# Kernel tuning notes

Hardware: AMD Instinct MI355X
Metric: run time of the kernel (lower is better)

## Reference

```python
import jax, jax.numpy as jnp
import numpy as np

NUM_NODES = 1_000_000
MEM = 128
NODE_F = 172
EDGE_F = 172
EMB = 128
DECAY = 0.1
B = 16384


def setup_inputs() -> dict:
    key = jax.random.key(0)
    ks = jax.random.split(key, 32)
    g = lambda k, sh, s=0.05: (s * jax.random.normal(k, sh)).astype(jnp.float32)
    inp = {
        "src_ids": jax.random.randint(ks[0], (B,), 0, NUM_NODES),
        "dst_ids": jax.random.randint(ks[1], (B,), 0, NUM_NODES),
        "src_features": g(ks[2], (B, NODE_F), 1.0),
        "dst_features": g(ks[3], (B, NODE_F), 1.0),
        "timestamps": jax.random.uniform(ks[4], (B,), jnp.float32),
        "edge_features": g(ks[5], (B, EDGE_F), 1.0),
        # persistent state (pre-populated so decay math is non-trivial)
        "memory0": g(ks[6], (NUM_NODES, MEM), 1.0),
        "last_update0": jax.random.uniform(ks[7], (NUM_NODES,), jnp.float32),
        # edge_embedding
        "W_edge": g(ks[8], (EDGE_F, MEM)), "b_edge": jnp.zeros((MEM,), jnp.float32),
        # message_processor: Linear(MEM,MEM) -> relu -> Linear(MEM,MEM)
        "W_mp1": g(ks[9], (MEM, MEM)), "b_mp1": jnp.zeros((MEM,), jnp.float32),
        "W_mp2": g(ks[10], (MEM, MEM)), "b_mp2": jnp.zeros((MEM,), jnp.float32),
        # GRUCell(MEM, MEM), torch layout [3*MEM, MEM] (r,z,n)
        "W_ih": g(ks[11], (3 * MEM, MEM)), "W_hh": g(ks[12], (3 * MEM, MEM)),
        "b_ih": jnp.zeros((3 * MEM,), jnp.float32), "b_hh": jnp.zeros((3 * MEM,), jnp.float32),
        # node_embedding
        "W_node": g(ks[13], (NODE_F, MEM)), "b_node": jnp.zeros((MEM,), jnp.float32),
        # embedding_projection: Linear(2*MEM, EMB) -> relu -> Linear(EMB, EMB)
        "W_p1": g(ks[14], (2 * MEM, EMB)), "b_p1": jnp.zeros((EMB,), jnp.float32),
        "W_p2": g(ks[15], (EMB, EMB)), "b_p2": jnp.zeros((EMB,), jnp.float32),
        # link_predictor: Linear(2*EMB, EMB) -> relu -> Linear(EMB, 1) -> sigmoid
        "W_l1": g(ks[16], (2 * EMB, EMB)), "b_l1": jnp.zeros((EMB,), jnp.float32),
        "W_l2": g(ks[17], (EMB, 1)), "b_l2": jnp.zeros((1,), jnp.float32),
    }
    return inp


def _gru_cell(x, h, W_ih, W_hh, b_ih, b_hh):
    gi = x @ W_ih.T + b_ih
    gh = h @ W_hh.T + b_hh
    i_r, i_z, i_n = jnp.split(gi, 3, axis=-1)
    h_r, h_z, h_n = jnp.split(gh, 3, axis=-1)
    r = jax.nn.sigmoid(i_r + h_r)
    z = jax.nn.sigmoid(i_z + h_z)
    n = jnp.tanh(i_n + r * h_n)
    return (1.0 - z) * n + z * h


def reference(src_ids, dst_ids, src_features, dst_features, timestamps, edge_features,
              memory0, last_update0,
              W_edge, b_edge, W_mp1, b_mp1, W_mp2, b_mp2,
              W_ih, W_hh, b_ih, b_hh, W_node, b_node,
              W_p1, b_p1, W_p2, b_p2, W_l1, b_l1, W_l2, b_l2):
    pos = jnp.arange(B, dtype=jnp.int32)

    def update_memory(memory, last_update, ids, messages, ts):
        # batched version of the torch per-row GRU loop: current memory is
        ids = jnp.clip(ids, 0, NUM_NODES - 1)
        proc = jax.nn.relu(messages @ W_mp1 + b_mp1) @ W_mp2 + b_mp2
        dt = jnp.maximum(ts - last_update[ids], 0.0)
        cur = memory[ids] * jnp.exp(-DECAY * dt)[:, None]          # decayed get_memory
        new = _gru_cell(proc, cur, W_ih, W_hh, b_ih, b_hh)          # [B, MEM]
        last_occ = jnp.full((NUM_NODES,), -1, jnp.int32).at[ids].max(pos)
        win = last_occ[ids] == pos
        wids = jnp.where(win, ids, NUM_NODES)                       # OOB rows dropped
        memory = memory.at[wids].set(new, mode="drop")
        last_update = last_update.at[wids].set(ts, mode="drop")
        # torch does updates under no_grad into non-trainable Parameters
        return jax.lax.stop_gradient(memory), jax.lax.stop_gradient(last_update)

    def compute_embeddings(memory, last_update, ids, feats, ts):
        ids = jnp.clip(ids, 0, NUM_NODES - 1)
        dt = jnp.maximum(ts - last_update[ids], 0.0)
        score = jnp.exp(-DECAY * dt)
        mem = memory[ids] * score[:, None]       # get_memory (decayed)
        attended = mem * score[:, None]          # temporal_attention decays again (faithful)
        node_emb = feats @ W_node + b_node
        comb = jnp.concatenate([attended, node_emb], axis=1)
        emb = jax.nn.relu(comb @ W_p1 + b_p1) @ W_p2 + b_p2
        return emb, score

    edge_emb = edge_features @ W_edge + b_edge
    memory, last_update = update_memory(memory0, last_update0, src_ids, edge_emb, timestamps)
    memory, last_update = update_memory(memory, last_update, dst_ids, edge_emb, timestamps)

    src_emb, src_score = compute_embeddings(memory, last_update, src_ids, src_features, timestamps)
    dst_emb, dst_score = compute_embeddings(memory, last_update, dst_ids, dst_features, timestamps)

    link = jnp.concatenate([src_emb, dst_emb], axis=1)
    link_probs = jax.nn.sigmoid(jax.nn.relu(link @ W_l1 + b_l1) @ W_l2 + b_l2)  # [B, 1]
    return link_probs, src_score, dst_score
```

## Files before the change

### kernel.cpp

```cpp
#include <hip/hip_runtime.h>
#include <hip/hip_bf16.h>

#define B_ROWS 16384
#define NODE_F 172
#define MEMD 128
#define NN 1000000

typedef __bf16 bf16;
typedef __bf16 bf16x8 __attribute__((ext_vector_type(8)));
typedef float f32x4 __attribute__((ext_vector_type(4)));

#define W_EDGE_O 0
#define W_MP1_O  24576
#define W_MP2_O  40960
#define W_IH_O   57344
#define W_HH_O   106496
#define W_NODE_O 155648
#define W_P1_O   180224
#define W_P2_O   212992
#define W_L1_O   229376
#define W_TOTAL  262144

__device__ __forceinline__ f32x4 mfma16(bf16x8 a, bf16x8 b, f32x4 c) {
    return __builtin_amdgcn_mfma_f32_16x16x32_bf16(a, b, c, 0, 0, 0);
}

__device__ __forceinline__ int clampid(int id) {
    return id < 0 ? 0 : (id > NN - 1 ? NN - 1 : id);
}

__device__ __forceinline__ float sigmoidf_(float x) {
    return 1.f / (1.f + __expf(-x));
}

__device__ __forceinline__ float tanhf_(float x) {
    return 1.f - 2.f / (__expf(2.f * x) + 1.f);
}

template<int NT, int KSTEPS>
__device__ __forceinline__ void gemm_wave(const bf16* Alds, int lda,
                                          const bf16* Bw, int ldb,
                                          f32x4* acc)
{
    int lane = threadIdx.x & 63;
    int p = lane & 15, q = lane >> 4;
    const bf16* ap  = Alds + p * lda + q * 8;
    const bf16* bp0 = Bw + (long)p * ldb + q * 8;
#pragma unroll
    for (int kt = 0; kt < KSTEPS; ++kt) {
        bf16x8 a = *(const bf16x8*)(ap + kt * 32);
#pragma unroll
        for (int j = 0; j < NT; ++j) {
            bf16x8 b = *(const bf16x8*)(bp0 + (long)j * 16 * ldb + kt * 32);
            acc[j] = mfma16(a, b, acc[j]);
        }
    }
}

__global__ __launch_bounds__(256) void prep_kernel(
    const float* __restrict__ W_edge, const float* __restrict__ W_mp1,
    const float* __restrict__ W_mp2, const float* __restrict__ W_ih,
    const float* __restrict__ W_hh, const float* __restrict__ W_node,
    const float* __restrict__ W_p1, const float* __restrict__ W_p2,
    const float* __restrict__ W_l1,
    int* __restrict__ occS, int* __restrict__ occD, bf16* __restrict__ wb)
{
    int gid = blockIdx.x * 256 + threadIdx.x;
    if (gid < NN / 4) {
        int4 m1 = {-1, -1, -1, -1};
        ((int4*)occS)[gid] = m1;
        ((int4*)occD)[gid] = m1;
    }
    int t = gid;
    if (t < W_TOTAL) {
        float v;
        if (t < W_MP1_O)      { int u = t;            int n = u / 192, k = u % 192; v = (k < NODE_F) ? W_edge[k * 128 + n] : 0.f; }
        else if (t < W_MP2_O) { int u = t - W_MP1_O;  int n = u / 128, k = u % 128; v = W_mp1[k * 128 + n]; }
        else if (t < W_IH_O)  { int u = t - W_MP2_O;  int n = u / 128, k = u % 128; v = W_mp2[k * 128 + n]; }
        else if (t < W_HH_O)  { int u = t - W_IH_O;   v = W_ih[u]; }
        else if (t < W_NODE_O){ int u = t - W_HH_O;   v = W_hh[u]; }
        else if (t < W_P1_O)  { int u = t - W_NODE_O; int n = u / 192, k = u % 192; v = (k < NODE_F) ? W_node[k * 128 + n] : 0.f; }
        else if (t < W_P2_O)  { int u = t - W_P1_O;   int n = u / 256, k = u % 256; v = W_p1[k * 128 + n]; }
        else if (t < W_L1_O)  { int u = t - W_P2_O;   int n = u / 128, k = u % 128; v = W_p2[k * 128 + n]; }
        else                  { int u = t - W_L1_O;   int n = u / 256, k = u % 256; v = W_l1[k * 128 + n]; }
        wb[t] = (bf16)v;
    }
}

__global__ __launch_bounds__(256) void proc_kernel(
    const float* __restrict__ edgef, const bf16* __restrict__ wb,
    const float* __restrict__ b_edge, const float* __restrict__ b_mp1,
    const float* __restrict__ b_mp2, const int* __restrict__ src_ids,
    const int* __restrict__ dst_ids, int* __restrict__ occS,
    int* __restrict__ occD, bf16* __restrict__ procB)
{
    __shared__ bf16 A0[64 * 200];
    __shared__ bf16 A1[64 * 136];
    __shared__ bf16 A2[64 * 136];
    int tid = threadIdx.x;
    long row0 = (long)blockIdx.x * 64;
    if (tid < 64) {
        int rid = (int)row0 + tid;
        atomicMax(&occS[clampid(src_ids[rid])], rid);
        atomicMax(&occD[clampid(dst_ids[rid])], rid);
    }
    {
        int r0 = tid >> 6, c0 = tid & 63;
        for (int r = r0; r < 64; r += 4)
            for (int c = c0; c < 192; c += 64)
                A0[r * 200 + c] = (c < NODE_F) ? (bf16)edgef[(row0 + r) * NODE_F + c] : (bf16)0.f;
    }
    __syncthreads();
    int w = tid >> 6, lane = tid & 63, p = lane & 15, q = lane >> 4;
    f32x4 acc[8];
    for (int j = 0; j < 8; ++j) acc[j] = (f32x4){0.f, 0.f, 0.f, 0.f};
    gemm_wave<8, 6>(A0 + (w * 16) * 200, 200, wb + W_EDGE_O, 192, acc);
    for (int j = 0; j < 8; ++j) {
        int col = j * 16 + p;
        float bb = b_edge[col];
        for (int v = 0; v < 4; ++v)
            A1[(w * 16 + q * 4 + v) * 136 + col] = (bf16)(acc[j][v] + bb);
    }
    __syncthreads();
    for (int j = 0; j < 8; ++j) acc[j] = (f32x4){0.f, 0.f, 0.f, 0.f};
    gemm_wave<8, 4>(A1 + (w * 16) * 136, 136, wb + W_MP1_O, 128, acc);
    for (int j = 0; j < 8; ++j) {
        int col = j * 16 + p;
        float bb = b_mp1[col];
        for (int v = 0; v < 4; ++v)
            A2[(w * 16 + q * 4 + v) * 136 + col] = (bf16)fmaxf(acc[j][v] + bb, 0.f);
    }
    __syncthreads();
    for (int j = 0; j < 8; ++j) acc[j] = (f32x4){0.f, 0.f, 0.f, 0.f};
    gemm_wave<8, 4>(A2 + (w * 16) * 136, 136, wb + W_MP2_O, 128, acc);
    for (int j = 0; j < 8; ++j) {
        int col = j * 16 + p;
        float bb = b_mp2[col];
        for (int v = 0; v < 4; ++v)
            procB[(row0 + w * 16 + q * 4 + v) * 128 + col] = (bf16)(acc[j][v] + bb);
    }
}

__global__ __launch_bounds__(256) void gru_kernel(
    const int* __restrict__ ids, const float* __restrict__ ts,
    const bf16* __restrict__ procB, const float* __restrict__ memory,
    const float* __restrict__ last_update, const int* __restrict__ occPrev,
    const float* __restrict__ newmemPrev, const bf16* __restrict__ wb,
    const float* __restrict__ b_ih, const float* __restrict__ b_hh,
    float* __restrict__ newmemOut, int round)
{
    __shared__ bf16 Ap[16 * 136];
    __shared__ bf16 Ac[16 * 136];
    __shared__ float curF[16 * 128];
    __shared__ float sA[16 * 384];
    __shared__ float sB[16 * 384];
    __shared__ float sc_s[16];
    __shared__ const float* rowp_s[16];
    int tid = threadIdx.x;
    int rb = blockIdx.x * 16;
    if (tid < 16) {
        int rid = rb + tid;
        int id = clampid(ids[rid]);
        const float* rowp = &memory[(long)id * MEMD];
        float lu = last_update[id];
        if (round) {
            int tg = occPrev[id];
            if (tg >= 0) { rowp = &newmemPrev[(long)tg * MEMD]; lu = ts[tg]; }
        }
        float dtv = fmaxf(ts[rid] - lu, 0.f);
        sc_s[tid] = __expf(-0.1f * dtv);
        rowp_s[tid] = rowp;
    }
    __syncthreads();
    {
        int r = tid >> 4, c8 = tid & 15;
        *(bf16x8*)&Ap[r * 136 + c8 * 8] = *(const bf16x8*)&procB[(long)(rb + r) * 128 + c8 * 8];
        float s = sc_s[r];
        f32x4 v0 = *(const f32x4*)(rowp_s[r] + c8 * 8);
        f32x4 v1 = *(const f32x4*)(rowp_s[r] + c8 * 8 + 4);
        v0.x *= s; v0.y *= s; v0.z *= s; v0.w *= s;
        v1.x *= s; v1.y *= s; v1.z *= s; v1.w *= s;
        *(f32x4*)&curF[r * 128 + c8 * 8] = v0;
        *(f32x4*)&curF[r * 128 + c8 * 8 + 4] = v1;
        bf16x8 cb;
        cb[0] = (bf16)v0.x; cb[1] = (bf16)v0.y; cb[2] = (bf16)v0.z; cb[3] = (bf16)v0.w;
        cb[4] = (bf16)v1.x; cb[5] = (bf16)v1.y; cb[6] = (bf16)v1.z; cb[7] = (bf16)v1.w;
        *(bf16x8*)&Ac[r * 136 + c8 * 8] = cb;
    }
    __syncthreads();
    int w = tid >> 6, lane = tid & 63, p = lane & 15, q = lane >> 4;
#pragma unroll
    for (int j = 0; j < 12; ++j) {
        int cidx = w * 12 + j;
        bool is_gi = cidx < 24;
        int nt = is_gi ? cidx : cidx - 24;
        const bf16* Al = (is_gi ? Ap : Ac) + p * 136 + q * 8;
        const bf16* Bw = wb + (is_gi ? W_IH_O : W_HH_O) + (long)(nt * 16 + p) * 128 + q * 8;
        f32x4 acc = (f32x4){0.f, 0.f, 0.f, 0.f};
#pragma unroll
        for (int kt = 0; kt < 4; ++kt) {
            bf16x8 a = *(const bf16x8*)(Al + kt * 32);
            bf16x8 b = *(const bf16x8*)(Bw + kt * 32);
            acc = mfma16(a, b, acc);
        }
        float* S = is_gi ? sA : sB;
        int col = nt * 16 + p;
        for (int v = 0; v < 4; ++v) S[(q * 4 + v) * 384 + col] = acc[v];
    }
    __syncthreads();
    for (int idx = tid; idx < 16 * 128; idx += 256) {
        int r = idx >> 7, c = idx & 127;
        float ir = sA[r * 384 + c]        + b_ih[c];
        float iz = sA[r * 384 + 128 + c]  + b_ih[128 + c];
        float in_ = sA[r * 384 + 256 + c] + b_ih[256 + c];
        float hr = sB[r * 384 + c]        + b_hh[c];
        float hz = sB[r * 384 + 128 + c]  + b_hh[128 + c];
        float hn = sB[r * 384 + 256 + c]  + b_hh[256 + c];
        float rg = sigmoidf_(ir + hr);
        float zg = sigmoidf_(iz + hz);
        float ng = tanhf_(in_ + rg * hn);
        float h = curF[r * 128 + c];
        newmemOut[(long)(rb + r) * 128 + c] = (1.f - zg) * ng + zg * h;
    }
}

__global__ __launch_bounds__(256) void emb_kernel(
    const int* __restrict__ src_ids, const int* __restrict__ dst_ids,
    const float* __restrict__ src_feat, const float* __restrict__ dst_feat,
    const float* __restrict__ ts, const float* __restrict__ memory,
    const float* __restrict__ last_update, const int* __restrict__ occS,
    const int* __restrict__ occD, const float* __restrict__ newmemS,
    const float* __restrict__ newmemD, const bf16* __restrict__ wb,
    const float* __restrict__ b_node, const float* __restrict__ b_p1,
    const float* __restrict__ b_p2, bf16* __restrict__ embS,
    bf16* __restrict__ embD, float* __restrict__ dout)
{
    int side = blockIdx.y;
    const int* ids = side ? dst_ids : src_ids;
    const float* feats = side ? dst_feat : src_feat;
    bf16* embOut = side ? embD : embS;
    __shared__ bf16 A0[64 * 200];
    __shared__ bf16 Comb[64 * 264];
    __shared__ bf16 A2[64 * 136];
    __shared__ float sc_s[64];
    __shared__ const float* rowp_s[64];
    int tid = threadIdx.x;
    long row0 = (long)blockIdx.x * 64;
    if (tid < 64) {
        int rid = (int)row0 + tid;
        int id = clampid(ids[rid]);
        const float* rowp = &memory[(long)id * MEMD];
        float lu = last_update[id];
        int tgD = occD[id], tgS = occS[id];
        if (tgD >= 0)      { rowp = &newmemD[(long)tgD * MEMD]; lu = ts[tgD]; }
        else if (tgS >= 0) { rowp = &newmemS[(long)tgS * MEMD]; lu = ts[tgS]; }
        float dtv = fmaxf(ts[rid] - lu, 0.f);
        float sc = __expf(-0.1f * dtv);
        sc_s[tid] = sc; rowp_s[tid] = rowp;
        dout[B_ROWS + side * B_ROWS + rid] = sc;
    }
    {
        int r0 = tid >> 6, c0 = tid & 63;
        for (int r = r0; r < 64; r += 4)
            for (int c = c0; c < 192; c += 64)
                A0[r * 200 + c] = (c < NODE_F) ? (bf16)feats[(row0 + r) * NODE_F + c] : (bf16)0.f;
    }
    __syncthreads();
    {
        for (int idx = tid; idx < 64 * 16; idx += 256) {
            int r = idx >> 4, c8 = idx & 15;
            float s = sc_s[r]; s = s * s;
            f32x4 v0 = *(const f32x4*)(rowp_s[r] + c8 * 8);
            f32x4 v1 = *(const f32x4*)(rowp_s[r] + c8 * 8 + 4);
            bf16x8 cb;
            cb[0] = (bf16)(v0.x * s); cb[1] = (bf16)(v0.y * s);
            cb[2] = (bf16)(v0.z * s); cb[3] = (bf16)(v0.w * s);
            cb[4] = (bf16)(v1.x * s); cb[5] = (bf16)(v1.y * s);
            cb[6] = (bf16)(v1.z * s); cb[7] = (bf16)(v1.w * s);
            *(bf16x8*)&Comb[r * 264 + c8 * 8] = cb;
        }
    }
    __syncthreads();
    int w = tid >> 6, lane = tid & 63, p = lane & 15, q = lane >> 4;
    f32x4 acc[8];
    for (int j = 0; j < 8; ++j) acc[j] = (f32x4){0.f, 0.f, 0.f, 0.f};
    gemm_wave<8, 6>(A0 + (w * 16) * 200, 200, wb + W_NODE_O, 192, acc);
    for (int j = 0; j < 8; ++j) {
        int col = j * 16 + p;
        float bb = b_node[col];
        for (int v = 0; v < 4; ++v)
            Comb[(w * 16 + q * 4 + v) * 264 + 128 + col] = (bf16)(acc[j][v] + bb);
    }
    __syncthreads();
    for (int j = 0; j < 8; ++j) acc[j] = (f32x4){0.f, 0.f, 0.f, 0.f};
    gemm_wave<8, 8>(Comb + (w * 16) * 264, 264, wb + W_P1_O, 256, acc);
    for (int j = 0; j < 8; ++j) {
        int col = j * 16 + p;
        float bb = b_p1[col];
        for (int v = 0; v < 4; ++v)
            A2[(w * 16 + q * 4 + v) * 136 + col] = (bf16)fmaxf(acc[j][v] + bb, 0.f);
    }
    __syncthreads();
    for (int j = 0; j < 8; ++j) acc[j] = (f32x4){0.f, 0.f, 0.f, 0.f};
    gemm_wave<8, 4>(A2 + (w * 16) * 136, 136, wb + W_P2_O, 128, acc);
    for (int j = 0; j < 8; ++j) {
        int col = j * 16 + p;
        float bb = b_p2[col];
        for (int v = 0; v < 4; ++v)
            embOut[(row0 + w * 16 + q * 4 + v) * 128 + col] = (bf16)(acc[j][v] + bb);
    }
}

__global__ __launch_bounds__(256) void link_kernel(
    const bf16* __restrict__ embS, const bf16* __restrict__ embD,
    const bf16* __restrict__ wb, const float* __restrict__ b_l1,
    const float* __restrict__ W_l2, const float* __restrict__ b_l2,
    float* __restrict__ out)
{
    __shared__ bf16 A[64 * 264];
    __shared__ float H[64 * 132];
    int tid = threadIdx.x;
    long row0 = (long)blockIdx.x * 64;
    for (int g = tid; g < 64 * 32; g += 256) {
        int r = g >> 5, c8 = g & 31;
        const bf16* src = (c8 < 16) ? &embS[(row0 + r) * 128 + c8 * 8]
                                    : &embD[(row0 + r) * 128 + (c8 - 16) * 8];
        *(bf16x8*)&A[r * 264 + c8 * 8] = *(const bf16x8*)src;
    }
    __syncthreads();
    int w = tid >> 6, lane = tid & 63, p = lane & 15, q = lane >> 4;
    f32x4 acc[8];
    for (int j = 0; j < 8; ++j) acc[j] = (f32x4){0.f, 0.f, 0.f, 0.f};
    gemm_wave<8, 8>(A + (w * 16) * 264, 264, wb + W_L1_O, 256, acc);
    for (int j = 0; j < 8; ++j) {
        int col = j * 16 + p;
        float bb = b_l1[col];
        for (int v = 0; v < 4; ++v)
            H[(w * 16 + q * 4 + v) * 132 + col] = fmaxf(acc[j][v] + bb, 0.f);
    }
    __syncthreads();
    if (tid < 64) {
        float a = b_l2[0];
        for (int c = 0; c < 128; ++c) a += H[tid * 132 + c] * W_l2[c];
        out[row0 + tid] = sigmoidf_(a);
    }
}

extern "C" void kernel_launch(void* const* d_in, const int* in_sizes, int n_in,
                              void* d_out, int out_size, void* d_ws, size_t ws_size,
                              hipStream_t stream)
{
    const int*   src_ids  = (const int*)d_in[0];
    const int*   dst_ids  = (const int*)d_in[1];
    const float* src_feat = (const float*)d_in[2];
    const float* dst_feat = (const float*)d_in[3];
    const float* ts       = (const float*)d_in[4];
    const float* edgef    = (const float*)d_in[5];
    const float* memory   = (const float*)d_in[6];
    const float* last_update = (const float*)d_in[7];
    const float* W_edge = (const float*)d_in[8],  *b_edge = (const float*)d_in[9];
    const float* W_mp1  = (const float*)d_in[10], *b_mp1  = (const float*)d_in[11];
    const float* W_mp2  = (const float*)d_in[12], *b_mp2  = (const float*)d_in[13];
    const float* W_ih   = (const float*)d_in[14], *W_hh   = (const float*)d_in[15];
    const float* b_ih   = (const float*)d_in[16], *b_hh   = (const float*)d_in[17];
    const float* W_node = (const float*)d_in[18], *b_node = (const float*)d_in[19];
    const float* W_p1   = (const float*)d_in[20], *b_p1   = (const float*)d_in[21];
    const float* W_p2   = (const float*)d_in[22], *b_p2   = (const float*)d_in[23];
    const float* W_l1   = (const float*)d_in[24], *b_l1   = (const float*)d_in[25];
    const float* W_l2   = (const float*)d_in[26], *b_l2   = (const float*)d_in[27];

    char* ws = (char*)d_ws;
    int*   occS     = (int*)ws;
    int*   occD     = (int*)(ws + 4000000);
    bf16*  wb       = (bf16*)(ws + 8000000);
    bf16*  procB    = (bf16*)(ws + 8524288);
    float* newmemS  = (float*)(ws + 12718592);
    float* newmemD  = (float*)(ws + 21107200);
    bf16*  embS     = (bf16*)(ws + 29495808);
    bf16*  embD     = (bf16*)(ws + 33690112);
    float* dout     = (float*)d_out;

    prep_kernel<<<1024, 256, 0, stream>>>(W_edge, W_mp1, W_mp2, W_ih, W_hh,
                                          W_node, W_p1, W_p2, W_l1, occS, occD, wb);
    proc_kernel<<<256, 256, 0, stream>>>(edgef, wb, b_edge, b_mp1, b_mp2,
                                         src_ids, dst_ids, occS, occD, procB);
    gru_kernel<<<1024, 256, 0, stream>>>(src_ids, ts, procB, memory, last_update,
                                         occS, newmemS, wb, b_ih, b_hh, newmemS, 0);
    gru_kernel<<<1024, 256, 0, stream>>>(dst_ids, ts, procB, memory, last_update,
                                         occS, newmemS, wb, b_ih, b_hh, newmemD, 1);
    emb_kernel<<<dim3(256, 2), 256, 0, stream>>>(src_ids, dst_ids, src_feat, dst_feat,
                                                 ts, memory, last_update, occS, occD,
                                                 newmemS, newmemD, wb,
                                                 b_node, b_p1, b_p2, embS, embD, dout);
    link_kernel<<<256, 256, 0, stream>>>(embS, embD, wb, b_l1, W_l2, b_l2, dout);
}
```

Baseline: 778.2 us.

## Fuse message processing with source GRU and embeddings with link predictor

Merges the message MLP with the source-side GRU update, and the two embedding passes with the link predictor, cutting six launches to four. Each wave now owns its 16-row slab end to end, so block barriers become compiler-only fences. The GRU gates are fused into register epilogues instead of being staged through shared-memory score buffers. Smaller 128-thread blocks with more of them raise occupancy, at the cost of recomputing decay scores and reading weights per wave.

```diff
diff --git a/kernel.cpp b/kernel.cpp
--- a/kernel.cpp
+++ b/kernel.cpp
@@ -37,6 +37,8 @@
     return 1.f - 2.f / (__expf(2.f * x) + 1.f);
 }
 
+__device__ __forceinline__ void wavefence() { asm volatile("" ::: "memory"); }
+
 template<int NT, int KSTEPS>
 __device__ __forceinline__ void gemm_wave(const bf16* Alds, int lda,
                                           const bf16* Bw, int ldb,
@@ -53,6 +55,53 @@
         for (int j = 0; j < NT; ++j) {
             bf16x8 b = *(const bf16x8*)(bp0 + (long)j * 16 * ldb + kt * 32);
             acc[j] = mfma16(a, b, acc[j]);
+        }
+    }
+}
+
+template<int KSTEPS>
+__device__ __forceinline__ void gru_tiles(
+    const bf16* ApSlab, const bf16* AcSlab, int lda,
+    const bf16* wih, const bf16* whh,
+    const float* __restrict__ b_ih, const float* __restrict__ b_hh,
+    const float* const* hrow, const float* s4,
+    float* __restrict__ outBase)
+{
+    int lane = threadIdx.x & 63;
+    int p = lane & 15, q = lane >> 4;
+    const bf16* ap = ApSlab + p * lda + q * 8;
+    const bf16* ac = AcSlab + p * lda + q * 8;
+#pragma unroll
+    for (int j = 0; j < 8; ++j) {
+        int col = j * 16 + p;
+        const bf16* br = wih + (long)col * 128 + q * 8;
+        const bf16* bz = br + 128 * 128;
+        const bf16* bn = bz + 128 * 128;
+        const bf16* cr = whh + (long)col * 128 + q * 8;
+        const bf16* cz = cr + 128 * 128;
+        const bf16* cn = cz + 128 * 128;
+        f32x4 air = {0.f,0.f,0.f,0.f}, aiz = {0.f,0.f,0.f,0.f}, ain = {0.f,0.f,0.f,0.f};
+        f32x4 ahr = {0.f,0.f,0.f,0.f}, ahz = {0.f,0.f,0.f,0.f}, ahn = {0.f,0.f,0.f,0.f};
+#pragma unroll
+        for (int kt = 0; kt < KSTEPS; ++kt) {
+            bf16x8 a1 = *(const bf16x8*)(ap + kt * 32);
+            bf16x8 a2 = *(const bf16x8*)(ac + kt * 32);
+            air = mfma16(a1, *(const bf16x8*)(br + kt * 32), air);
+            aiz = mfma16(a1, *(const bf16x8*)(bz + kt * 32), aiz);
+            ain = mfma16(a1, *(const bf16x8*)(bn + kt * 32), ain);
+            ahr = mfma16(a2, *(const bf16x8*)(cr + kt * 32), ahr);
+            ahz = mfma16(a2, *(const bf16x8*)(cz + kt * 32), ahz);
+            ahn = mfma16(a2, *(const bf16x8*)(cn + kt * 32), ahn);
+        }
+        float bir = b_ih[col], biz = b_ih[128 + col], bin = b_ih[256 + col];
+        float bhr = b_hh[col], bhz = b_hh[128 + col], bhn = b_hh[256 + col];
+#pragma unroll
+        for (int v = 0; v < 4; ++v) {
+            float rg = sigmoidf_(air[v] + bir + ahr[v] + bhr);
+            float zg = sigmoidf_(aiz[v] + biz + ahz[v] + bhz);
+            float ng = tanhf_(ain[v] + bin + rg * (ahn[v] + bhn));
+            float h  = hrow[v][col] * s4[v];
+            outBase[(q * 4 + v) * MEMD + col] = (1.f - zg) * ng + zg * h;
         }
     }
 }
@@ -87,144 +136,157 @@
     }
 }
 
-__global__ __launch_bounds__(256) void proc_kernel(
-    const float* __restrict__ edgef, const bf16* __restrict__ wb,
+__global__ __launch_bounds__(128) void pgs_kernel(
+    const int* __restrict__ src_ids, const int* __restrict__ dst_ids,
+    const float* __restrict__ ts, const float* __restrict__ edgef,
+    const float* __restrict__ memory, const float* __restrict__ last_update,
+    const bf16* __restrict__ wb,
     const float* __restrict__ b_edge, const float* __restrict__ b_mp1,
-    const float* __restrict__ b_mp2, const int* __restrict__ src_ids,
-    const int* __restrict__ dst_ids, int* __restrict__ occS,
-    int* __restrict__ occD, bf16* __restrict__ procB)
-{
-    __shared__ bf16 A0[64 * 200];
-    __shared__ bf16 A1[64 * 136];
-    __shared__ bf16 A2[64 * 136];
+    const float* __restrict__ b_mp2, const float* __restrict__ b_ih,
+    const float* __restrict__ b_hh,
+    int* __restrict__ occS, int* __restrict__ occD,
+    bf16* __restrict__ procB, float* __restrict__ newmemS)
+{
+    __shared__ bf16 A0[32 * 200];
+    __shared__ bf16 A1[32 * 136];
+    __shared__ bf16 Ac[32 * 136];
     int tid = threadIdx.x;
-    long row0 = (long)blockIdx.x * 64;
-    if (tid < 64) {
+    long row0 = (long)blockIdx.x * 32;
+    if (tid < 32) {
         int rid = (int)row0 + tid;
         atomicMax(&occS[clampid(src_ids[rid])], rid);
         atomicMax(&occD[clampid(dst_ids[rid])], rid);
     }
-    {
-        int r0 = tid >> 6, c0 = tid & 63;
-        for (int r = r0; r < 64; r += 4)
-            for (int c = c0; c < 192; c += 64)
-                A0[r * 200 + c] = (c < NODE_F) ? (bf16)edgef[(row0 + r) * NODE_F + c] : (bf16)0.f;
-    }
-    __syncthreads();
     int w = tid >> 6, lane = tid & 63, p = lane & 15, q = lane >> 4;
+    int r0 = w * 16;
+    const float4* ef = (const float4*)edgef;
+    for (int i = lane; i < 16 * 43; i += 64) {
+        int r = i / 43, c4 = i - r * 43;
+        float4 v = ef[(row0 + r0 + r) * 43 + c4];
+        bf16* d = &A0[(r0 + r) * 200 + c4 * 4];
+        d[0] = (bf16)v.x; d[1] = (bf16)v.y; d[2] = (bf16)v.z; d[3] = (bf16)v.w;
+    }
+    for (int i = lane; i < 16 * 20; i += 64) {
+        int r = i / 20, c = i - r * 20;
+        A0[(r0 + r) * 200 + 172 + c] = (bf16)0.f;
+    }
+    wavefence();
     f32x4 acc[8];
     for (int j = 0; j < 8; ++j) acc[j] = (f32x4){0.f, 0.f, 0.f, 0.f};
-    gemm_wave<8, 6>(A0 + (w * 16) * 200, 200, wb + W_EDGE_O, 192, acc);
+    gemm_wave<8, 6>(A0 + r0 * 200, 200, wb + W_EDGE_O, 192, acc);
     for (int j = 0; j < 8; ++j) {
-        int col = j * 16 + p;
-        float bb = b_edge[col];
-        for (int v = 0; v < 4; ++v)
-            A1[(w * 16 + q * 4 + v) * 136 + col] = (bf16)(acc[j][v] + bb);
-    }
-    __syncthreads();
+        int col = j * 16 + p; float bb = b_edge[col];
+#pragma unroll
+        for (int v = 0; v < 4; ++v) A1[(r0 + q * 4 + v) * 136 + col] = (bf16)(acc[j][v] + bb);
+    }
+    wavefence();
     for (int j = 0; j < 8; ++j) acc[j] = (f32x4){0.f, 0.f, 0.f, 0.f};
-    gemm_wave<8, 4>(A1 + (w * 16) * 136, 136, wb + W_MP1_O, 128, acc);
+    gemm_wave<8, 4>(A1 + r0 * 136, 136, wb + W_MP1_O, 128, acc);
+    bf16* myA2 = A0 + r0 * 200;
     for (int j = 0; j < 8; ++j) {
-        int col = j * 16 + p;
-        float bb = b_mp1[col];
-        for (int v = 0; v < 4; ++v)
-            A2[(w * 16 + q * 4 + v) * 136 + col] = (bf16)fmaxf(acc[j][v] + bb, 0.f);
-    }
-    __syncthreads();
+        int col = j * 16 + p; float bb = b_mp1[col];
+#pragma unroll
+        for (int v = 0; v < 4; ++v) myA2[(q * 4 + v) * 136 + col] = (bf16)fmaxf(acc[j][v] + bb, 0.f);
+    }
+    wavefence();
     for (int j = 0; j < 8; ++j) acc[j] = (f32x4){0.f, 0.f, 0.f, 0.f};
-    gemm_wave<8, 4>(A2 + (w * 16) * 136, 136, wb + W_MP2_O, 128, acc);
+    gemm_wave<8, 4>(myA2, 136, wb + W_MP2_O, 128, acc);
+    bf16* myAp = A1 + r0 * 136;
     for (int j = 0; j < 8; ++j) {
-        int col = j * 16 + p;
-        float bb = b_mp2[col];
-        for (int v = 0; v < 4; ++v)
-            procB[(row0 + w * 16 + q * 4 + v) * 128 + col] = (bf16)(acc[j][v] + bb);
-    }
-}
-
-__global__ __launch_bounds__(256) void gru_kernel(
-    const int* __restrict__ ids, const float* __restrict__ ts,
+        int col = j * 16 + p; float bb = b_mp2[col];
+#pragma unroll
+        for (int v = 0; v < 4; ++v) {
+            float pv = acc[j][v] + bb;
+            myAp[(q * 4 + v) * 136 + col] = (bf16)pv;
+            procB[(row0 + r0 + q * 4 + v) * MEMD + col] = (bf16)pv;
+        }
+    }
+    for (int i = lane; i < 256; i += 64) {
+        int r = i >> 4, c8 = i & 15;
+        int rid = (int)row0 + r0 + r;
+        int id = clampid(src_ids[rid]);
+        float lu = last_update[id];
+        float s = __expf(-0.1f * fmaxf(ts[rid] - lu, 0.f));
+        const float* rp = memory + (long)id * MEMD + c8 * 8;
+        f32x4 v0 = *(const f32x4*)rp;
+        f32x4 v1 = *(const f32x4*)(rp + 4);
+        bf16x8 cb;
+        cb[0] = (bf16)(v0.x * s); cb[1] = (bf16)(v0.y * s);
+        cb[2] = (bf16)(v0.z * s); cb[3] = (bf16)(v0.w * s);
+        cb[4] = (bf16)(v1.x * s); cb[5] = (bf16)(v1.y * s);
+        cb[6] = (bf16)(v1.z * s); cb[7] = (bf16)(v1.w * s);
+        *(bf16x8*)&Ac[(r0 + r) * 136 + c8 * 8] = cb;
+    }
+    wavefence();
+    const float* hrow[4]; float s4[4];
+#pragma unroll
+    for (int v = 0; v < 4; ++v) {
+        int rid = (int)row0 + r0 + q * 4 + v;
+        int id = clampid(src_ids[rid]);
+        float lu = last_update[id];
+        s4[v] = __expf(-0.1f * fmaxf(ts[rid] - lu, 0.f));
+        hrow[v] = memory + (long)id * MEMD;
+    }
+    gru_tiles<4>(myAp, Ac + r0 * 136, 136, wb + W_IH_O, wb + W_HH_O,
+                 b_ih, b_hh, hrow, s4, newmemS + (row0 + r0) * MEMD);
+}
+
+__global__ __launch_bounds__(128) void grud_kernel(
+    const int* __restrict__ dst_ids, const float* __restrict__ ts,
     const bf16* __restrict__ procB, const float* __restrict__ memory,
-    const float* __restrict__ last_update, const int* __restrict__ occPrev,
-    const float* __restrict__ newmemPrev, const bf16* __restrict__ wb,
+    const float* __restrict__ last_update, const int* __restrict__ occS,
+    const float* __restrict__ newmemS, const bf16* __restrict__ wb,
     const float* __restrict__ b_ih, const float* __restrict__ b_hh,
-    float* __restrict__ newmemOut, int round)
-{
-    __shared__ bf16 Ap[16 * 136];
-    __shared__ bf16 Ac[16 * 136];
-    __shared__ float curF[16 * 128];
-    __shared__ float sA[16 * 384];
-    __shared__ float sB[16 * 384];
-    __shared__ float sc_s[16];
-    __shared__ const float* rowp_s[16];
+    float* __restrict__ newmemD)
+{
+    __shared__ bf16 Ap[32 * 136];
+    __shared__ bf16 Ac[32 * 136];
     int tid = threadIdx.x;
-    int rb = blockIdx.x * 16;
-    if (tid < 16) {
-        int rid = rb + tid;
-        int id = clampid(ids[rid]);
-        const float* rowp = &memory[(long)id * MEMD];
-        float lu = last_update[id];
-        if (round) {
-            int tg = occPrev[id];
-            if (tg >= 0) { rowp = &newmemPrev[(long)tg * MEMD]; lu = ts[tg]; }
-        }
-        float dtv = fmaxf(ts[rid] - lu, 0.f);
-        sc_s[tid] = __expf(-0.1f * dtv);
-        rowp_s[tid] = rowp;
-    }
-    __syncthreads();
-    {
-        int r = tid >> 4, c8 = tid & 15;
-        *(bf16x8*)&Ap[r * 136 + c8 * 8] = *(const bf16x8*)&procB[(long)(rb + r) * 128 + c8 * 8];
-        float s = sc_s[r];
-        f32x4 v0 = *(const f32x4*)(rowp_s[r] + c8 * 8);
-        f32x4 v1 = *(const f32x4*)(rowp_s[r] + c8 * 8 + 4);
-        v0.x *= s; v0.y *= s; v0.z *= s; v0.w *= s;
-        v1.x *= s; v1.y *= s; v1.z *= s; v1.w *= s;
-        *(f32x4*)&curF[r * 128 + c8 * 8] = v0;
-        *(f32x4*)&curF[r * 128 + c8 * 8 + 4] = v1;
+    long row0 = (long)blockIdx.x * 32;
+    int w = tid >> 6, lane = tid & 63, p = lane & 15, q = lane >> 4;
+    int r0 = w * 16;
+    for (int i = lane; i < 256; i += 64) {
+        int r = i >> 4, c8 = i & 15;
+        *(bf16x8*)&Ap[(r0 + r) * 136 + c8 * 8] =
+            *(const bf16x8*)&procB[(row0 + r0 + r) * MEMD + c8 * 8];
+    }
+    for (int i = lane; i < 256; i += 64) {
+        int r = i >> 4, c8 = i & 15;
+        int rid = (int)row0 + r0 + r;
+        int id = clampid(dst_ids[rid]);
+        int tg = occS[id];
+        const float* rp; float lu;
+        if (tg >= 0) { rp = newmemS + (long)tg * MEMD; lu = ts[tg]; }
+        else         { rp = memory + (long)id * MEMD;  lu = last_update[id]; }
+        float s = __expf(-0.1f * fmaxf(ts[rid] - lu, 0.f));
+        const float* rpp = rp + c8 * 8;
+        f32x4 v0 = *(const f32x4*)rpp;
+        f32x4 v1 = *(const f32x4*)(rpp + 4);
         bf16x8 cb;
-        cb[0] = (bf16)v0.x; cb[1] = (bf16)v0.y; cb[2] = (bf16)v0.z; cb[3] = (bf16)v0.w;
-        cb[4] = (bf16)v1.x; cb[5] = (bf16)v1.y; cb[6] = (bf16)v1.z; cb[7] = (bf16)v1.w;
-        *(bf16x8*)&Ac[r * 136 + c8 * 8] = cb;
-    }
-    __syncthreads();
-    int w = tid >> 6, lane = tid & 63, p = lane & 15, q = lane >> 4;
-#pragma unroll
-    for (int j = 0; j < 12; ++j) {
-        int cidx = w * 12 + j;
-        bool is_gi = cidx < 24;
-        int nt = is_gi ? cidx : cidx - 24;
-        const bf16* Al = (is_gi ? Ap : Ac) + p * 136 + q * 8;
-        const bf16* Bw = wb + (is_gi ? W_IH_O : W_HH_O) + (long)(nt * 16 + p) * 128 + q * 8;
-        f32x4 acc = (f32x4){0.f, 0.f, 0.f, 0.f};
-#pragma unroll
-        for (int kt = 0; kt < 4; ++kt) {
-            bf16x8 a = *(const bf16x8*)(Al + kt * 32);
-            bf16x8 b = *(const bf16x8*)(Bw + kt * 32);
-            acc = mfma16(a, b, acc);
-        }
-        float* S = is_gi ? sA : sB;
-        int col = nt * 16 + p;
-        for (int v = 0; v < 4; ++v) S[(q * 4 + v) * 384 + col] = acc[v];
-    }
-    __syncthreads();
-    for (int idx = tid; idx < 16 * 128; idx += 256) {
-        int r = idx >> 7, c = idx & 127;
-        float ir = sA[r * 384 + c]        + b_ih[c];
-        float iz = sA[r * 384 + 128 + c]  + b_ih[128 + c];
-        float in_ = sA[r * 384 + 256 + c] + b_ih[256 + c];
-        float hr = sB[r * 384 + c]        + b_hh[c];
-        float hz = sB[r * 384 + 128 + c]  + b_hh[128 + c];
-        float hn = sB[r * 384 + 256 + c]  + b_hh[256 + c];
-        float rg = sigmoidf_(ir + hr);
-        float zg = sigmoidf_(iz + hz);
-        float ng = tanhf_(in_ + rg * hn);
-        float h = curF[r * 128 + c];
-        newmemOut[(long)(rb + r) * 128 + c] = (1.f - zg) * ng + zg * h;
-    }
-}
-
-__global__ __launch_bounds__(256) void emb_kernel(
+        cb[0] = (bf16)(v0.x * s); cb[1] = (bf16)(v0.y * s);
+        cb[2] = (bf16)(v0.z * s); cb[3] = (bf16)(v0.w * s);
+        cb[4] = (bf16)(v1.x * s); cb[5] = (bf16)(v1.y * s);
+        cb[6] = (bf16)(v1.z * s); cb[7] = (bf16)(v1.w * s);
+        *(bf16x8*)&Ac[(r0 + r) * 136 + c8 * 8] = cb;
+    }
+    wavefence();
+    const float* hrow[4]; float s4[4];
+#pragma unroll
+    for (int v = 0; v < 4; ++v) {
+        int rid = (int)row0 + r0 + q * 4 + v;
+        int id = clampid(dst_ids[rid]);
+        int tg = occS[id];
+        const float* rp; float lu;
+        if (tg >= 0) { rp = newmemS + (long)tg * MEMD; lu = ts[tg]; }
+        else         { rp = memory + (long)id * MEMD;  lu = last_update[id]; }
+        s4[v] = __expf(-0.1f * fmaxf(ts[rid] - lu, 0.f));
+        hrow[v] = rp;
+    }
+    gru_tiles<4>(Ap + r0 * 136, Ac + r0 * 136, 136, wb + W_IH_O, wb + W_HH_O,
+                 b_ih, b_hh, hrow, s4, newmemD + (row0 + r0) * MEMD);
+}
+
+__global__ __launch_bounds__(128) void embl_kernel(
     const int* __restrict__ src_ids, const int* __restrict__ dst_ids,
     const float* __restrict__ src_feat, const float* __restrict__ dst_feat,
     const float* __restrict__ ts, const float* __restrict__ memory,
@@ -232,117 +294,105 @@
     const int* __restrict__ occD, const float* __restrict__ newmemS,
     const float* __restrict__ newmemD, const bf16* __restrict__ wb,
     const float* __restrict__ b_node, const float* __restrict__ b_p1,
-    const float* __restrict__ b_p2, bf16* __restrict__ embS,
-    bf16* __restrict__ embD, float* __restrict__ dout)
-{
-    int side = blockIdx.y;
-    const int* ids = side ? dst_ids : src_ids;
-    const float* feats = side ? dst_feat : src_feat;
-    bf16* embOut = side ? embD : embS;
-    __shared__ bf16 A0[64 * 200];
-    __shared__ bf16 Comb[64 * 264];
-    __shared__ bf16 A2[64 * 136];
-    __shared__ float sc_s[64];
-    __shared__ const float* rowp_s[64];
+    const float* __restrict__ b_p2, const float* __restrict__ b_l1,
+    const float* __restrict__ W_l2, const float* __restrict__ b_l2,
+    float* __restrict__ dout)
+{
+    __shared__ bf16 A0[32 * 200];
+    __shared__ bf16 Comb[32 * 264];
+    __shared__ bf16 E[32 * 264];
     int tid = threadIdx.x;
-    long row0 = (long)blockIdx.x * 64;
-    if (tid < 64) {
-        int rid = (int)row0 + tid;
-        int id = clampid(ids[rid]);
-        const float* rowp = &memory[(long)id * MEMD];
-        float lu = last_update[id];
-        int tgD = occD[id], tgS = occS[id];
-        if (tgD >= 0)      { rowp = &newmemD[(long)tgD * MEMD]; lu = ts[tgD]; }
-        else if (tgS >= 0) { rowp = &newmemS[(long)tgS * MEMD]; lu = ts[tgS]; }
-        float dtv = fmaxf(ts[rid] - lu, 0.f);
-        float sc = __expf(-0.1f * dtv);
-        sc_s[tid] = sc; rowp_s[tid] = rowp;
-        dout[B_ROWS + side * B_ROWS + rid] = sc;
-    }
-    {
-        int r0 = tid >> 6, c0 = tid & 63;
-        for (int r = r0; r < 64; r += 4)
-            for (int c = c0; c < 192; c += 64)
-                A0[r * 200 + c] = (c < NODE_F) ? (bf16)feats[(row0 + r) * NODE_F + c] : (bf16)0.f;
-    }
-    __syncthreads();
-    {
-        for (int idx = tid; idx < 64 * 16; idx += 256) {
-            int r = idx >> 4, c8 = idx & 15;
-            float s = sc_s[r]; s = s * s;
-            f32x4 v0 = *(const f32x4*)(rowp_s[r] + c8 * 8);
-            f32x4 v1 = *(const f32x4*)(rowp_s[r] + c8 * 8 + 4);
+    long row0 = (long)blockIdx.x * 32;
+    int w = tid >> 6, lane = tid & 63, p = lane & 15, q = lane >> 4;
+    int r0 = w * 16;
+    f32x4 acc[8];
+    for (int side = 0; side < 2; ++side) {
+        const int* ids = side ? dst_ids : src_ids;
+        const float4* ft = (const float4*)(side ? dst_feat : src_feat);
+        wavefence();
+        for (int i = lane; i < 16 * 43; i += 64) {
+            int r = i / 43, c4 = i - r * 43;
+            float4 v = ft[(row0 + r0 + r) * 43 + c4];
+            bf16* d = &A0[(r0 + r) * 200 + c4 * 4];
+            d[0] = (bf16)v.x; d[1] = (bf16)v.y; d[2] = (bf16)v.z; d[3] = (bf16)v.w;
+        }
+        for (int i = lane; i < 16 * 20; i += 64) {
+            int r = i / 20, c = i - r * 20;
+            A0[(r0 + r) * 200 + 172 + c] = (bf16)0.f;
+        }
+        for (int i = lane; i < 256; i += 64) {
+            int r = i >> 4, c8 = i & 15;
+            int rid = (int)row0 + r0 + r;
+            int id = clampid(ids[rid]);
+            int tgD = occD[id], tgS = occS[id];
+            const float* rp; float lu;
+            if (tgD >= 0)      { rp = newmemD + (long)tgD * MEMD; lu = ts[tgD]; }
+            else if (tgS >= 0) { rp = newmemS + (long)tgS * MEMD; lu = ts[tgS]; }
+            else               { rp = memory + (long)id * MEMD;   lu = last_update[id]; }
+            float sc = __expf(-0.1f * fmaxf(ts[rid] - lu, 0.f));
+            if (c8 == 0) dout[B_ROWS + side * B_ROWS + rid] = sc;
+            float ss = sc * sc;
+            const float* rpp = rp + c8 * 8;
+            f32x4 v0 = *(const f32x4*)rpp;
+            f32x4 v1 = *(const f32x4*)(rpp + 4);
             bf16x8 cb;
-            cb[0] = (bf16)(v0.x * s); cb[1] = (bf16)(v0.y * s);
-            cb[2] = (bf16)(v0.z * s); cb[3] = (bf16)(v0.w * s);
-            cb[4] = (bf16)(v1.x * s); cb[5] = (bf16)(v1.y * s);
-            cb[6] = (bf16)(v1.z * s); cb[7] = (bf16)(v1.w * s);
-            *(bf16x8*)&Comb[r * 264 + c8 * 8] = cb;
-        }
-    }
-    __syncthreads();
-    int w = tid >> 6, lane = tid & 63, p = lane & 15, q = lane >> 4;
-    f32x4 acc[8];
+            cb[0] = (bf16)(v0.x * ss); cb[1] = (bf16)(v0.y * ss);
+            cb[2] = (bf16)(v0.z * ss); cb[3] = (bf16)(v0.w * ss);
+            cb[4] = (bf16)(v1.x * ss); cb[5] = (bf16)(v1.y * ss);
+            cb[6] = (bf16)(v1.z * ss); cb[7] = (bf16)(v1.w * ss);
+            *(bf16x8*)&Comb[(r0 + r) * 264 + c8 * 8] = cb;
+        }
+        wavefence();
+        for (int j = 0; j < 8; ++j) acc[j] = (f32x4){0.f, 0.f, 0.f, 0.f};
+        gemm_wave<8, 6>(A0 + r0 * 200, 200, wb + W_NODE_O, 192, acc);
+        for (int j = 0; j < 8; ++j) {
+            int col = j * 16 + p; float bb = b_node[col];
+#pragma unroll
+            for (int v = 0; v < 4; ++v)
+                Comb[(r0 + q * 4 + v) * 264 + 128 + col] = (bf16)(acc[j][v] + bb);
+        }
+        wavefence();
+        for (int j = 0; j < 8; ++j) acc[j] = (f32x4){0.f, 0.f, 0.f, 0.f};
+        gemm_wave<8, 8>(Comb + r0 * 264, 264, wb + W_P1_O, 256, acc);
+        bf16* myA2 = A0 + r0 * 200;
+        for (int j = 0; j < 8; ++j) {
+            int col = j * 16 + p; float bb = b_p1[col];
+#pragma unroll
+            for (int v = 0; v < 4; ++v)
+                myA2[(q * 4 + v) * 136 + col] = (bf16)fmaxf(acc[j][v] + bb, 0.f);
+        }
+        wavefence();
+        for (int j = 0; j < 8; ++j) acc[j] = (f32x4){0.f, 0.f, 0.f, 0.f};
+        gemm_wave<8, 4>(myA2, 136, wb + W_P2_O, 128, acc);
+        for (int j = 0; j < 8; ++j) {
+            int col = j * 16 + p; float bb = b_p2[col];
+#pragma unroll
+            for (int v = 0; v < 4; ++v)
+                E[(r0 + q * 4 + v) * 264 + side * 128 + col] = (bf16)(acc[j][v] + bb);
+        }
+    }
+    wavefence();
     for (int j = 0; j < 8; ++j) acc[j] = (f32x4){0.f, 0.f, 0.f, 0.f};
-    gemm_wave<8, 6>(A0 + (w * 16) * 200, 200, wb + W_NODE_O, 192, acc);
-    for (int j = 0; j < 8; ++j) {
-        int col = j * 16 + p;
-        float bb = b_node[col];
-        for (int v = 0; v < 4; ++v)
-            Comb[(w * 16 + q * 4 + v) * 264 + 128 + col] = (bf16)(acc[j][v] + bb);
-    }
-    __syncthreads();
-    for (int j = 0; j < 8; ++j) acc[j] = (f32x4){0.f, 0.f, 0.f, 0.f};
-    gemm_wave<8, 8>(Comb + (w * 16) * 264, 264, wb + W_P1_O, 256, acc);
-    for (int j = 0; j < 8; ++j) {
-        int col = j * 16 + p;
-        float bb = b_p1[col];
-        for (int v = 0; v < 4; ++v)
-            A2[(w * 16 + q * 4 + v) * 136 + col] = (bf16)fmaxf(acc[j][v] + bb, 0.f);
-    }
-    __syncthreads();
-    for (int j = 0; j < 8; ++j) acc[j] = (f32x4){0.f, 0.f, 0.f, 0.f};
-    gemm_wave<8, 4>(A2 + (w * 16) * 136, 136, wb + W_P2_O, 128, acc);
-    for (int j = 0; j < 8; ++j) {
-        int col = j * 16 + p;
-        float bb = b_p2[col];
-        for (int v = 0; v < 4; ++v)
-            embOut[(row0 + w * 16 + q * 4 + v) * 128 + col] = (bf16)(acc[j][v] + bb);
-    }
-}
-
-__global__ __launch_bounds__(256) void link_kernel(
-    const bf16* __restrict__ embS, const bf16* __restrict__ embD,
-    const bf16* __restrict__ wb, const float* __restrict__ b_l1,
-    const float* __restrict__ W_l2, const float* __restrict__ b_l2,
-    float* __restrict__ out)
-{
-    __shared__ bf16 A[64 * 264];
-    __shared__ float H[64 * 132];
-    int tid = threadIdx.x;
-    long row0 = (long)blockIdx.x * 64;
-    for (int g = tid; g < 64 * 32; g += 256) {
-        int r = g >> 5, c8 = g & 31;
-        const bf16* src = (c8 < 16) ? &embS[(row0 + r) * 128 + c8 * 8]
-                                    : &embD[(row0 + r) * 128 + (c8 - 16) * 8];
-        *(bf16x8*)&A[r * 264 + c8 * 8] = *(const bf16x8*)src;
-    }
-    __syncthreads();
-    int w = tid >> 6, lane = tid & 63, p = lane & 15, q = lane >> 4;
-    f32x4 acc[8];
-    for (int j = 0; j < 8; ++j) acc[j] = (f32x4){0.f, 0.f, 0.f, 0.f};
-    gemm_wave<8, 8>(A + (w * 16) * 264, 264, wb + W_L1_O, 256, acc);
+    gemm_wave<8, 8>(E + r0 * 264, 264, wb + W_L1_O, 256, acc);
+    float part[4] = {0.f, 0.f, 0.f, 0.f};
+#pragma unroll
     for (int j = 0; j < 8; ++j) {
         int col = j * 16 + p;
         float bb = b_l1[col];
+        float wl = W_l2[col];
+#pragma unroll
+        for (int v = 0; v < 4; ++v) part[v] += fmaxf(acc[j][v] + bb, 0.f) * wl;
+    }
+#pragma unroll
+    for (int m = 1; m < 16; m <<= 1) {
+#pragma unroll
+        for (int v = 0; v < 4; ++v) part[v] += __shfl_xor(part[v], m);
+    }
+    if (p == 0) {
+        float bl = b_l2[0];
+#pragma unroll
         for (int v = 0; v < 4; ++v)
-            H[(w * 16 + q * 4 + v) * 132 + col] = fmaxf(acc[j][v] + bb, 0.f);
-    }
-    __syncthreads();
-    if (tid < 64) {
-        float a = b_l2[0];
-        for (int c = 0; c < 128; ++c) a += H[tid * 132 + c] * W_l2[c];
-        out[row0 + tid] = sigmoidf_(a);
+            dout[row0 + r0 + q * 4 + v] = sigmoidf_(part[v] + bl);
     }
 }
 
@@ -376,21 +426,17 @@
     bf16*  procB    = (bf16*)(ws + 8524288);
     float* newmemS  = (float*)(ws + 12718592);
     float* newmemD  = (float*)(ws + 21107200);
-    bf16*  embS     = (bf16*)(ws + 29495808);
-    bf16*  embD     = (bf16*)(ws + 33690112);
     float* dout     = (float*)d_out;
 
     prep_kernel<<<1024, 256, 0, stream>>>(W_edge, W_mp1, W_mp2, W_ih, W_hh,
                                           W_node, W_p1, W_p2, W_l1, occS, occD, wb);
-    proc_kernel<<<256, 256, 0, stream>>>(edgef, wb, b_edge, b_mp1, b_mp2,
-                                         src_ids, dst_ids, occS, occD, procB);
-    gru_kernel<<<1024, 256, 0, stream>>>(src_ids, ts, procB, memory, last_update,
-                                         occS, newmemS, wb, b_ih, b_hh, newmemS, 0);
-    gru_kernel<<<1024, 256, 0, stream>>>(dst_ids, ts, procB, memory, last_update,
-                                         occS, newmemS, wb, b_ih, b_hh, newmemD, 1);
-    emb_kernel<<<dim3(256, 2), 256, 0, stream>>>(src_ids, dst_ids, src_feat, dst_feat,
-                                                 ts, memory, last_update, occS, occD,
-                                                 newmemS, newmemD, wb,
-                                                 b_node, b_p1, b_p2, embS, embD, dout);
-    link_kernel<<<256, 256, 0, stream>>>(embS, embD, wb, b_l1, W_l2, b_l2, dout);
-}
+    pgs_kernel<<<512, 128, 0, stream>>>(src_ids, dst_ids, ts, edgef, memory, last_update,
+                                        wb, b_edge, b_mp1, b_mp2, b_ih, b_hh,
+                                        occS, occD, procB, newmemS);
+    grud_kernel<<<512, 128, 0, stream>>>(dst_ids, ts, procB, memory, last_update,
+                                         occS, newmemS, wb, b_ih, b_hh, newmemD);
+    embl_kernel<<<512, 128, 0, stream>>>(src_ids, dst_ids, src_feat, dst_feat,
+                                         ts, memory, last_update, occS, occD,
+                                         newmemS, newmemD, wb,
+                                         b_node, b_p1, b_p2, b_l1, W_l2, b_l2, dout);
+}
```

Result: slower. 800.1 us (+2.8%).
